# Kernel tuning notes

Hardware: AMD Instinct MI355X
Metric: run time of the kernel (lower is better)

## Reference

```python
import jax, jax.numpy as jnp
import numpy as np

K = 16        # neighbors
M = 4         # repeat count
EPS = 1e-5    # BatchNorm eps (torch default)


def setup_inputs() -> dict:
    key = jax.random.key(0)
    k1, k2, k3, k4 = jax.random.split(key, 4)
    B, N, C, Fe = 8, 8192, 64, 32  # Fe = int(channels * dim_expand)
    return {
        "xyz": jax.random.normal(k1, (B, N, 3), dtype=jnp.float32),
        "feat": jax.random.normal(k2, (B, C, N), dtype=jnp.float32),
        "bn_gamma": jnp.ones((C,), jnp.float32),
        "bn_beta": jnp.zeros((C,), jnp.float32),
        "Wg": jax.random.normal(k3, (Fe, C + 3), jnp.float32) * 0.1,   # g_func weight [out, in]
        "Wh": jax.random.normal(k4, (C, M * Fe), jnp.float32) * 0.1,   # h_func weight [out, in]
    }


def reference(xyz, feat, bn_gamma, bn_beta, Wg, Wh):
    # xyz: [B, N, 3], feat: [B, C, N]
    # --- bn0: training-mode BatchNorm1d over channel dim (stats over B, N) ---
    mean = feat.mean(axis=(0, 2), keepdims=True)
    var = feat.var(axis=(0, 2), keepdims=True)
    fbn = bn_gamma[None, :, None] * (feat - mean) * jax.lax.rsqrt(var + EPS) + bn_beta[None, :, None]

    # --- g_func on concat(feat_bn, xyz^T) -> feat0 [B, N, Fe] ---
    cat = jnp.concatenate([fbn, jnp.transpose(xyz, (0, 2, 1))], axis=1)  # [B, C+3, N]
    feat0 = jnp.einsum('bcn,ec->bne', cat, Wg)                           # [B, N, Fe]

    # --- bknn: pairwise squared distances, top-k of -dist (computed once) ---
    xx = jnp.sum(xyz * xyz, axis=-1)                                     # [B, N]
    dist = xx[:, :, None] - 2.0 * jnp.einsum('bnd,bmd->bnm', xyz, xyz) + xx[:, None, :]
    _, idx = jax.lax.top_k(-dist, K)                                     # [B, N, K] int32

    # --- gather neighbor features, max-pool over K ---
    group = jax.vmap(lambda f, i: f[i])(feat0, idx)                      # [B, N, K, Fe]
    gmax = group.max(axis=2)                                             # [B, N, Fe]
    rel = gmax - feat0                                                   # [B, N, Fe]

    # Original loop reuses cached idx and feat0 every iteration, so all M
    # concatenated blocks are identical -> tile along the feature dim.
    rel_rep = jnp.concatenate([rel] * M, axis=-1)                        # [B, N, M*Fe]

    # --- h_func -> output [B, C, N] ---
    out = jnp.einsum('bnf,cf->bcn', rel_rep, Wh)
    return out
```

## Files before the change

kernel.cpp:

```cpp
#include <hip/hip_runtime.h>
#include <math.h>

#define BB 8
#define NN 8192
#define CC 64
#define FE 32
#define KN 16
#define CP3 67
#define QPW 4
#define WPB 4
#define CAPQ 64
#define YB 32
#define ZB 32
#define NCELL (YB * ZB)

__device__ double g_part[BB * CC * 2];
__device__ float g_feat0[BB * NN * FE];
__device__ int   g_idx[BB * NN * KN];
__device__ float4 g_sorted[BB * NN];
__device__ int    g_sorig[BB * NN];
__device__ unsigned g_binoff[BB * (NCELL + 1)];

__device__ __forceinline__ int cbin(float v) {
    int bi = (int)((v + 4.5f) * (32.0f / 9.0f));
    if (bi < 0) bi = 0;
    if (bi > 31) bi = 31;
    return bi;
}
__device__ __forceinline__ float frz_xx(float x, float y, float z) {
    return __fmaf_rn(z, z, __fmaf_rn(y, y, __fmul_rn(x, x)));
}

__global__ __launch_bounds__(256) void k_bnstats(const float* __restrict__ feat) {
    int bc = blockIdx.x;
    const float* p = feat + (size_t)bc * NN;
    int tid = threadIdx.x;
    double s = 0.0, s2 = 0.0;
    for (int n = tid; n < NN; n += 256) {
        double v = (double)p[n];
        s += v; s2 += v * v;
    }
    __shared__ double sh[256], sh2[256];
    sh[tid] = s; sh2[tid] = s2;
    __syncthreads();
    for (int off = 128; off > 0; off >>= 1) {
        if (tid < off) { sh[tid] += sh[tid + off]; sh2[tid] += sh2[tid + off]; }
        __syncthreads();
    }
    if (tid == 0) {
        g_part[bc * 2]     = sh[0];
        g_part[bc * 2 + 1] = sh2[0];
    }
}

__global__ __launch_bounds__(1024) void k_zbin(const float* __restrict__ xyz) {
    __shared__ unsigned hist[NCELL];
    __shared__ unsigned scan[NCELL];
    __shared__ unsigned boff[NCELL + 1];
    int b = blockIdx.x;
    int tid = threadIdx.x;
    hist[tid] = 0;
    __syncthreads();
    const float* bx = xyz + (size_t)b * NN * 3;
    for (int n = tid; n < NN; n += 1024) {
        float y = bx[n * 3 + 1], z = bx[n * 3 + 2];
        atomicAdd(&hist[cbin(y) * ZB + cbin(z)], 1u);
    }
    __syncthreads();
    scan[tid] = hist[tid];
    __syncthreads();
    for (int off = 1; off < NCELL; off <<= 1) {
        unsigned add = (tid >= off) ? scan[tid - off] : 0u;
        __syncthreads();
        scan[tid] += add;
        __syncthreads();
    }
    if (tid == 0) boff[0] = 0;
    boff[tid + 1] = scan[tid];
    __syncthreads();
    hist[tid] = 0;
    g_binoff[b * (NCELL + 1) + tid + 1] = boff[tid + 1];
    if (tid == 0) g_binoff[b * (NCELL + 1)] = 0;
    __syncthreads();
    for (int n = tid; n < NN; n += 1024) {
        const float* p = bx + (size_t)n * 3;
        float x = p[0], y = p[1], z = p[2];
        int cell = cbin(y) * ZB + cbin(z);
        unsigned pos = boff[cell] + atomicAdd(&hist[cell], 1u);
        g_sorted[(size_t)b * NN + pos] = make_float4(x, y, z, frz_xx(x, y, z));
        g_sorig[(size_t)b * NN + pos] = n;
    }
}

__global__ __launch_bounds__(256) void k_feat0(const float* __restrict__ feat,
        const float* __restrict__ xyz, const float* __restrict__ Wg,
        const float* __restrict__ gamma, const float* __restrict__ beta) {
    __shared__ float scs[CC], shs[CC];
    __shared__ float wgs[CP3 * FE];
    __shared__ float bias0[FE];
    int tid = threadIdx.x;
    if (tid < CC) {
        double s = 0.0, s2 = 0.0;
        for (int bb2 = 0; bb2 < BB; ++bb2) {
            s  += g_part[((bb2 << 6) + tid) * 2];
            s2 += g_part[((bb2 << 6) + tid) * 2 + 1];
        }
        double inv = 1.0 / (double)(BB * NN);
        double mean = s * inv;
        double var = s2 * inv - mean * mean;
        float sc = gamma[tid] * (float)(1.0 / sqrt(var + (double)1e-5f));
        scs[tid] = sc;
        shs[tid] = beta[tid] - sc * (float)mean;
    }
    __syncthreads();
    for (int i = tid; i < CP3 * FE; i += 256) {
        int c = i >> 5, e = i & 31;
        float w = Wg[e * CP3 + c];
        if (c < CC) w *= scs[c];
        wgs[c * FE + e] = w;
    }
    if (tid < FE) {
        float sacc = 0.f;
        for (int c = 0; c < CC; ++c) sacc = fmaf(Wg[tid * CP3 + c], shs[c], sacc);
        bias0[tid] = sacc;
    }
    __syncthreads();
    int b = blockIdx.x >> 5;
    int n = ((blockIdx.x & 31) << 8) + tid;
    const float* pz = xyz + ((size_t)(b * NN + n)) * 3;
    float x = pz[0], y = pz[1], z = pz[2];

    float acc[FE];
    #pragma unroll
    for (int e = 0; e < FE; ++e) acc[e] = bias0[e];
    const float* fp = feat + (size_t)b * CC * NN + n;
    for (int c = 0; c < CC; ++c) {
        float v = fp[(size_t)c * NN];
        const float4* w4 = (const float4*)(wgs + c * FE);
        #pragma unroll
        for (int e0 = 0; e0 < 8; ++e0) {
            float4 w = w4[e0];
            acc[e0 * 4 + 0] = fmaf(w.x, v, acc[e0 * 4 + 0]);
            acc[e0 * 4 + 1] = fmaf(w.y, v, acc[e0 * 4 + 1]);
            acc[e0 * 4 + 2] = fmaf(w.z, v, acc[e0 * 4 + 2]);
            acc[e0 * 4 + 3] = fmaf(w.w, v, acc[e0 * 4 + 3]);
        }
    }
    #pragma unroll
    for (int d = 0; d < 3; ++d) {
        float v = (d == 0) ? x : ((d == 1) ? y : z);
        const float4* w4 = (const float4*)(wgs + (CC + d) * FE);
        #pragma unroll
        for (int e0 = 0; e0 < 8; ++e0) {
            float4 w = w4[e0];
            acc[e0 * 4 + 0] = fmaf(w.x, v, acc[e0 * 4 + 0]);
            acc[e0 * 4 + 1] = fmaf(w.y, v, acc[e0 * 4 + 1]);
            acc[e0 * 4 + 2] = fmaf(w.z, v, acc[e0 * 4 + 2]);
            acc[e0 * 4 + 3] = fmaf(w.w, v, acc[e0 * 4 + 3]);
        }
    }
    float4* outp = (float4*)(g_feat0 + ((size_t)(b * NN + n)) * FE);
    #pragma unroll
    for (int e0 = 0; e0 < 8; ++e0)
        outp[e0] = make_float4(acc[e0 * 4 + 0], acc[e0 * 4 + 1], acc[e0 * 4 + 2], acc[e0 * 4 + 3]);
}

__global__ __launch_bounds__(256) void k_knn() {
    __shared__ unsigned long long qbuf[WPB * CAPQ];
    int tid = threadIdx.x;
    int lane = tid & 63;
    int w = tid >> 6;
    int wid = blockIdx.x * WPB + w;
    int b = wid >> 11;
    int g = wid & 2047;
    const float4* S = g_sorted + (size_t)b * NN;
    const int* SO = g_sorig + (size_t)b * NN;
    const unsigned* BO = g_binoff + b * (NCELL + 1);
    unsigned long long lt = (1ull << lane) - 1ull;
    unsigned long long* pb = qbuf + w * CAPQ;

    #pragma unroll 1
    for (int i = 0; i < QPW; ++i) {
        int qrank = g + (i << 11);
        float4 qv = S[qrank];
        float qx = qv.x, qy = qv.y, qz = qv.z, qxx = qv.w;
        int qorig = SO[qrank];
        float tt = 0.053f * __expf(qxx * (1.0f / 3.0f));
        float t0 = tt > 3.f ? 3.f : tt;
        float tlo = 0.f, thi = 0.f;
        unsigned cnt = 0;

        for (int attempt = 0; attempt < 40; ++attempt) {
            cnt = 0;
            float R = __fsqrt_rn(t0 + 1e-3f) + 1e-3f;
            int ylo = cbin(qy - R), yhi = cbin(qy + R);
            int zlo = cbin(qz - R), zhi = cbin(qz + R);

            int yb = ylo;
            int p = (int)BO[yb * ZB + zlo];
            int hi = (int)BO[yb * ZB + zhi + 1];
            while (p >= hi && yb < yhi) {
                ++yb;
                p = (int)BO[yb * ZB + zlo];
                hi = (int)BO[yb * ZB + zhi + 1];
            }
            bool have = p < hi;
            int jc = 0; float4 cur; bool inc = false;
            if (have) {
                jc = p + lane; if (jc > hi - 1) jc = hi - 1;
                cur = S[jc];
                inc = (p + lane) < hi;
            }
            while (have) {
                int yb2 = yb, p2 = p + 64, hi2 = hi;
                while (p2 >= hi2 && yb2 < yhi) {
                    ++yb2;
                    p2 = (int)BO[yb2 * ZB + zlo];
                    hi2 = (int)BO[yb2 * ZB + zhi + 1];
                }
                bool have2 = p2 < hi2;
                int jn = jc; float4 nxt = cur; bool inn = false;
                if (have2) {
                    jn = p2 + lane; if (jn > hi2 - 1) jn = hi2 - 1;
                    nxt = S[jn];
                    inn = (p2 + lane) < hi2;
                }
                float dot = __fmaf_rn(qz, cur.z, __fmaf_rn(qy, cur.y, __fmul_rn(qx, cur.x)));
                float dist = __fadd_rn(__fmaf_rn(-2.f, dot, qxx), cur.w);
                bool pr = (dist <= t0) && inc;
                unsigned long long mask = __ballot(pr);
                if (mask) {
                    unsigned pos = cnt + (unsigned)__popcll(mask & lt);
                    if (pr && pos < CAPQ) {
                        int corig = SO[jc];
                        int db = __float_as_int(dist);
                        unsigned key = (unsigned)db ^ (unsigned)((db >> 31) | 0x80000000);
                        pb[pos] = ((unsigned long long)key << 32) | (unsigned)corig;
                    }
                    cnt += (unsigned)__popcll(mask);
                }
                yb = yb2; p = p2; hi = hi2; have = have2;
                jc = jn; cur = nxt; inc = inn;
            }
            if (cnt < KN) {
                tlo = t0;
                t0 = (thi > 0.f) ? __fsqrt_rn(tlo * thi) : t0 * 2.0f;
            } else if (cnt > CAPQ) {
                thi = t0;
                t0 = (tlo > 0.f) ? __fsqrt_rn(tlo * thi) : t0 * 0.5f;
            } else break;
        }

        unsigned tot = cnt > CAPQ ? CAPQ : cnt;
        unsigned long long e0 = ((unsigned)lane < tot) ? pb[lane] : ~0ull;
        unsigned rank0 = 0;
        for (unsigned jx = 0; jx < tot; ++jx) {
            unsigned long long v = pb[jx];
            rank0 += (v < e0) ? 1u : 0u;
        }
        if (((unsigned)lane < tot) && rank0 < KN)
            g_idx[(b * NN + qorig) * KN + rank0] = (int)(e0 & 0xffffffffull);
    }
}

__global__ __launch_bounds__(256) void k_out(const float* __restrict__ Wh,
        float* __restrict__ out) {
    __shared__ float whs[CC * FE];
    int tid = threadIdx.x;
    for (int i = tid; i < CC * FE; i += 256) {
        int c = i >> 5, e = i & 31;
        float s = 0.f;
        #pragma unroll
        for (int m = 0; m < 4; ++m) s += Wh[c * 128 + m * 32 + e];
        whs[i] = s;
    }
    __syncthreads();
    int b = blockIdx.x >> 5;
    int n = ((blockIdx.x & 31) << 8) + tid;
    const int* ip = g_idx + (size_t)(b * NN + n) * KN;
    const float4* f0 = (const float4*)(g_feat0 + (size_t)b * NN * FE);
    float gmax[FE];
    #pragma unroll
    for (int e = 0; e < FE; ++e) gmax[e] = -__builtin_inff();
    for (int k = 0; k < KN; ++k) {
        int id = ip[k] & (NN - 1);
        const float4* row = f0 + (size_t)id * 8;
        #pragma unroll
        for (int e0 = 0; e0 < 8; ++e0) {
            float4 v = row[e0];
            gmax[e0 * 4 + 0] = fmaxf(gmax[e0 * 4 + 0], v.x);
            gmax[e0 * 4 + 1] = fmaxf(gmax[e0 * 4 + 1], v.y);
            gmax[e0 * 4 + 2] = fmaxf(gmax[e0 * 4 + 2], v.z);
            gmax[e0 * 4 + 3] = fmaxf(gmax[e0 * 4 + 3], v.w);
        }
    }
    const float4* selfr = f0 + (size_t)n * 8;
    float rel[FE];
    #pragma unroll
    for (int e0 = 0; e0 < 8; ++e0) {
        float4 v = selfr[e0];
        rel[e0 * 4 + 0] = gmax[e0 * 4 + 0] - v.x;
        rel[e0 * 4 + 1] = gmax[e0 * 4 + 1] - v.y;
        rel[e0 * 4 + 2] = gmax[e0 * 4 + 2] - v.z;
        rel[e0 * 4 + 3] = gmax[e0 * 4 + 3] - v.w;
    }
    float* op = out + (size_t)b * CC * NN + n;
    for (int c = 0; c < CC; ++c) {
        const float4* w4 = (const float4*)(whs + c * FE);
        float s = 0.f;
        #pragma unroll
        for (int e0 = 0; e0 < 8; ++e0) {
            float4 w = w4[e0];
            s = fmaf(w.x, rel[e0 * 4 + 0], s);
            s = fmaf(w.y, rel[e0 * 4 + 1], s);
            s = fmaf(w.z, rel[e0 * 4 + 2], s);
            s = fmaf(w.w, rel[e0 * 4 + 3], s);
        }
        op[(size_t)c * NN] = s;
    }
}

extern "C" void kernel_launch(void* const* d_in, const int* in_sizes, int n_in,
                              void* d_out, int out_size, void* d_ws, size_t ws_size,
                              hipStream_t stream) {
    const float* xyz   = (const float*)d_in[0];
    const float* feat  = (const float*)d_in[1];
    const float* gamma = (const float*)d_in[2];
    const float* beta  = (const float*)d_in[3];
    const float* Wg    = (const float*)d_in[4];
    const float* Wh    = (const float*)d_in[5];
    float* out = (float*)d_out;
    (void)d_ws; (void)ws_size;

    hipLaunchKernelGGL(k_bnstats, dim3(512),  dim3(256),  0, stream, feat);
    hipLaunchKernelGGL(k_zbin,    dim3(8),    dim3(1024), 0, stream, xyz);
    hipLaunchKernelGGL(k_feat0,   dim3(256),  dim3(256),  0, stream, feat, xyz, Wg, gamma, beta);
    hipLaunchKernelGGL(k_knn,     dim3(4096), dim3(256),  0, stream);
    hipLaunchKernelGGL(k_out,     dim3(256),  dim3(256),  0, stream, Wh, out);
}
```

Measured before the change: 207.3 us.

## Trim z-range per y-row to circle cross-section and process two candidates per lane

For each y-row of the grid, the z-bin range is narrowed to the cross-section of the search sphere at that row, so fewer candidate points are scanned than with the full square z-window. The candidate scan loop also now processes two points per lane per iteration (128 per wave step), with two ballots and a combined prefix for buffer positions. This is meant to cut wasted distance evaluations and loop overhead in the kNN search, at the cost of extra per-row sqrt/bin math and higher register use from the doubled prefetch.

```diff
diff --git a/kernel.cpp b/kernel.cpp
--- a/kernel.cpp
+++ b/kernel.cpp
@@ -192,55 +192,93 @@
 
         for (int attempt = 0; attempt < 40; ++attempt) {
             cnt = 0;
-            float R = __fsqrt_rn(t0 + 1e-3f) + 1e-3f;
+            float tpe = t0 + 1e-3f;
+            float R = __fsqrt_rn(tpe) + 1e-3f;
             int ylo = cbin(qy - R), yhi = cbin(qy + R);
-            int zlo = cbin(qz - R), zhi = cbin(qz + R);
-
-            int yb = ylo;
-            int p = (int)BO[yb * ZB + zlo];
-            int hi = (int)BO[yb * ZB + zhi + 1];
+
+            int yb = ylo, p = 0, hi = 0;
+            {
+                float rowlo = 0.28125f * (float)yb - 4.5f;
+                float dy = fmaxf(0.f, fmaxf(rowlo - qy, qy - (rowlo + 0.28125f)));
+                float rz2 = tpe - dy * dy;
+                if (rz2 > 0.f) {
+                    float Rz = __fsqrt_rn(rz2) + 1e-3f;
+                    int zl = cbin(qz - Rz), zh = cbin(qz + Rz);
+                    p = (int)BO[yb * ZB + zl]; hi = (int)BO[yb * ZB + zh + 1];
+                }
+            }
             while (p >= hi && yb < yhi) {
                 ++yb;
-                p = (int)BO[yb * ZB + zlo];
-                hi = (int)BO[yb * ZB + zhi + 1];
+                float rowlo = 0.28125f * (float)yb - 4.5f;
+                float dy = fmaxf(0.f, fmaxf(rowlo - qy, qy - (rowlo + 0.28125f)));
+                float rz2 = tpe - dy * dy;
+                if (rz2 > 0.f) {
+                    float Rz = __fsqrt_rn(rz2) + 1e-3f;
+                    int zl = cbin(qz - Rz), zh = cbin(qz + Rz);
+                    p = (int)BO[yb * ZB + zl]; hi = (int)BO[yb * ZB + zh + 1];
+                } else { p = 0; hi = 0; }
             }
             bool have = p < hi;
-            int jc = 0; float4 cur; bool inc = false;
+            int jc0 = 0, jc1 = 0; bool in0 = false, in1 = false;
+            float4 c0, c1;
             if (have) {
-                jc = p + lane; if (jc > hi - 1) jc = hi - 1;
-                cur = S[jc];
-                inc = (p + lane) < hi;
+                int base = p + 2 * lane;
+                jc0 = base < hi ? base : hi - 1;
+                jc1 = base + 1 < hi ? base + 1 : hi - 1;
+                c0 = S[jc0]; c1 = S[jc1];
+                in0 = base < hi; in1 = base + 1 < hi;
             }
             while (have) {
-                int yb2 = yb, p2 = p + 64, hi2 = hi;
+                int yb2 = yb, p2 = p + 128, hi2 = hi;
                 while (p2 >= hi2 && yb2 < yhi) {
                     ++yb2;
-                    p2 = (int)BO[yb2 * ZB + zlo];
-                    hi2 = (int)BO[yb2 * ZB + zhi + 1];
+                    float rowlo = 0.28125f * (float)yb2 - 4.5f;
+                    float dy = fmaxf(0.f, fmaxf(rowlo - qy, qy - (rowlo + 0.28125f)));
+                    float rz2 = tpe - dy * dy;
+                    if (rz2 > 0.f) {
+                        float Rz = __fsqrt_rn(rz2) + 1e-3f;
+                        int zl = cbin(qz - Rz), zh = cbin(qz + Rz);
+                        p2 = (int)BO[yb2 * ZB + zl]; hi2 = (int)BO[yb2 * ZB + zh + 1];
+                    } else { p2 = 0; hi2 = 0; }
                 }
                 bool have2 = p2 < hi2;
-                int jn = jc; float4 nxt = cur; bool inn = false;
+                int jn0 = jc0, jn1 = jc1; bool inn0 = false, inn1 = false;
+                float4 n0 = c0, n1 = c1;
                 if (have2) {
-                    jn = p2 + lane; if (jn > hi2 - 1) jn = hi2 - 1;
-                    nxt = S[jn];
-                    inn = (p2 + lane) < hi2;
+                    int base = p2 + 2 * lane;
+                    jn0 = base < hi2 ? base : hi2 - 1;
+                    jn1 = base + 1 < hi2 ? base + 1 : hi2 - 1;
+                    n0 = S[jn0]; n1 = S[jn1];
+                    inn0 = base < hi2; inn1 = base + 1 < hi2;
                 }
-                float dot = __fmaf_rn(qz, cur.z, __fmaf_rn(qy, cur.y, __fmul_rn(qx, cur.x)));
-                float dist = __fadd_rn(__fmaf_rn(-2.f, dot, qxx), cur.w);
-                bool pr = (dist <= t0) && inc;
-                unsigned long long mask = __ballot(pr);
-                if (mask) {
-                    unsigned pos = cnt + (unsigned)__popcll(mask & lt);
-                    if (pr && pos < CAPQ) {
-                        int corig = SO[jc];
-                        int db = __float_as_int(dist);
+                float dot0 = __fmaf_rn(qz, c0.z, __fmaf_rn(qy, c0.y, __fmul_rn(qx, c0.x)));
+                float dist0 = __fadd_rn(__fmaf_rn(-2.f, dot0, qxx), c0.w);
+                float dot1 = __fmaf_rn(qz, c1.z, __fmaf_rn(qy, c1.y, __fmul_rn(qx, c1.x)));
+                float dist1 = __fadd_rn(__fmaf_rn(-2.f, dot1, qxx), c1.w);
+                bool pr0 = (dist0 <= t0) && in0;
+                bool pr1 = (dist1 <= t0) && in1;
+                unsigned long long m0 = __ballot(pr0);
+                unsigned long long m1 = __ballot(pr1);
+                if (m0 | m1) {
+                    unsigned n0c = (unsigned)__popcll(m0);
+                    unsigned pos0 = cnt + (unsigned)__popcll(m0 & lt);
+                    unsigned pos1 = cnt + n0c + (unsigned)__popcll(m1 & lt);
+                    if (pr0 && pos0 < CAPQ) {
+                        int corig = SO[jc0];
+                        int db = __float_as_int(dist0);
                         unsigned key = (unsigned)db ^ (unsigned)((db >> 31) | 0x80000000);
-                        pb[pos] = ((unsigned long long)key << 32) | (unsigned)corig;
+                        pb[pos0] = ((unsigned long long)key << 32) | (unsigned)corig;
                     }
-                    cnt += (unsigned)__popcll(mask);
+                    if (pr1 && pos1 < CAPQ) {
+                        int corig = SO[jc1];
+                        int db = __float_as_int(dist1);
+                        unsigned key = (unsigned)db ^ (unsigned)((db >> 31) | 0x80000000);
+                        pb[pos1] = ((unsigned long long)key << 32) | (unsigned)corig;
+                    }
+                    cnt += n0c + (unsigned)__popcll(m1);
                 }
                 yb = yb2; p = p2; hi = hi2; have = have2;
-                jc = jn; cur = nxt; inc = inn;
+                jc0 = jn0; jc1 = jn1; c0 = n0; c1 = n1; in0 = inn0; in1 = inn1;
             }
             if (cnt < KN) {
                 tlo = t0;
```

Result: faster. 201.0 us (median of 2 runs) (-3.0%).
